# Kernel optimization log

Measured on AMD Instinct MI355X. Metric: run time of the kernel, lower is better.

The kernel has to match this reference:

```python
import jax, jax.numpy as jnp
import numpy as np

B, T, N, C, H = 32, 50, 1024, 128, 64


def setup_inputs() -> dict:
    key = jax.random.key(0)
    ks = jax.random.split(key, 5)
    s_ih = 1.0 / np.sqrt(H)
    return {
        "chars": jax.random.normal(ks[0], (B, T, N, C), dtype=jnp.float32),
        "W_ih": jax.random.uniform(ks[1], (3 * H, C), minval=-s_ih, maxval=s_ih, dtype=jnp.float32),
        "W_hh": jax.random.uniform(ks[2], (3 * H, H), minval=-s_ih, maxval=s_ih, dtype=jnp.float32),
        "b_ih": jax.random.uniform(ks[3], (3 * H,), minval=-s_ih, maxval=s_ih, dtype=jnp.float32),
        "b_hh": jax.random.uniform(ks[4], (3 * H,), minval=-s_ih, maxval=s_ih, dtype=jnp.float32),
    }


def _gru_scan(chars, W_ih, W_hh, b_ih, b_hh):
    b, t, n, c = chars.shape
    h_dim = W_hh.shape[1]
    # (B,T,N,C) -> (T, B*N, C): every (batch, stock) pair is an independent sequence
    x = jnp.transpose(chars, (1, 0, 2, 3)).reshape(t, b * n, c)
    # precompute input projections for all steps: (T, B*N, 3H)
    gi = jnp.einsum("tbc,gc->tbg", x, W_ih) + b_ih

    def step(h, gi_t):
        gh = h @ W_hh.T + b_hh                      # (B*N, 3H)
        i_r, i_z, i_n = jnp.split(gi_t, 3, axis=-1)
        h_r, h_z, h_n = jnp.split(gh, 3, axis=-1)
        r = jax.nn.sigmoid(i_r + h_r)
        z = jax.nn.sigmoid(i_z + h_z)
        nn_ = jnp.tanh(i_n + r * h_n)
        h_new = (1.0 - z) * nn_ + z * h
        return h_new, None

    h0 = jnp.zeros((b * n, h_dim), dtype=chars.dtype)
    h_final, _ = jax.lax.scan(step, h0, gi)
    return h_final.reshape(b, n, h_dim)


def reference(chars, W_ih, W_hh, b_ih, b_hh):
    return _gru_scan(chars, W_ih, W_hh, b_ih, b_hh)
```

## Files before the change

kernel.cpp:

```cpp
#include <hip/hip_runtime.h>


typedef _Float16 half8 __attribute__((ext_vector_type(8)));
typedef float f32x4 __attribute__((ext_vector_type(4)));

constexpr int T_ = 50, N_ = 1024, C_ = 128, H_ = 64;
constexpr uint32_t WIH_OFF = 0;
constexpr uint32_t HT_OFF  = 49152;
constexpr int LDS_BYTES = 57344;

__global__ void prep_weights(const float* __restrict__ Wih, const float* __restrict__ Whh,
                             _Float16* __restrict__ w16) {
  int i = blockIdx.x * 256 + threadIdx.x;
  if (i < 192 * 128) w16[i] = (_Float16)Wih[i];
  if (i < 192 * 64)  w16[24576 + i] = (_Float16)Whh[i];
}

__device__ __forceinline__ float sigm(float x) {
  return __builtin_amdgcn_rcpf(1.f + __expf(-x));
}

__global__ __launch_bounds__(256, 2) void gru_phase(
    const float* __restrict__ x, const _Float16* __restrict__ w16,
    const float* __restrict__ bih, const float* __restrict__ bhh,
    float* __restrict__ out)
{
  __shared__ __align__(16) char lds[LDS_BYTES];
  const int tid = threadIdx.x;

  {
#pragma unroll
    for (int rep = 0; rep < 12; ++rep) {
      int i = tid + rep * 256;
      int row = i >> 4;
      uint32_t byte = ((uint32_t)i << 4) ^ ((uint32_t)(row & 7) << 4);
      *(half8*)(lds + WIH_OFF + byte) = *(const half8*)(w16 + i * 8);
    }
    half8 zz = {};
    *(half8*)(lds + HT_OFF + tid * 32)      = zz;
    *(half8*)(lds + HT_OFF + tid * 32 + 16) = zz;
  }
  __syncthreads();

  const int wv = tid >> 6, lane = tid & 63;
  const int c = lane & 15, g = lane >> 4;
  const int sw7 = c & 7;
  const uint32_t ht = HT_OFF + (uint32_t)wv * 2048;
  const int seq0 = blockIdx.x * 64 + wv * 16;
  const int b = seq0 >> 10, n0 = seq0 & (N_ - 1);

  const _Float16* whh = w16 + 24576;
  half8 wf[3][4][2];
#pragma unroll
  for (int gate = 0; gate < 3; ++gate)
#pragma unroll
    for (int jt = 0; jt < 4; ++jt)
#pragma unroll
      for (int ks2 = 0; ks2 < 2; ++ks2)
        wf[gate][jt][ks2] =
            *(const half8*)(whh + (gate * 64 + jt * 16 + c) * 64 + ks2 * 32 + g * 8);

  float br[4], bz[4], bin_[4], bhn_[4];
#pragma unroll
  for (int jt = 0; jt < 4; ++jt) {
    int j = jt * 16 + c;
    br[jt]   = bih[j] + bhh[j];
    bz[jt]   = bih[64 + j] + bhh[64 + j];
    bin_[jt] = bih[128 + j];
    bhn_[jt] = bhh[128 + j];
  }

  float hr[16];
#pragma unroll
  for (int i = 0; i < 16; ++i) hr[i] = 0.f;

  const float* xlane = x + ((size_t)b * T_ * N_ + n0 + c) * C_ + g * 8;
  const size_t stepstride = (size_t)N_ * C_;

#define WIHB(gate, jt, ks) \
  (*(const half8*)(lds + WIH_OFF + (uint32_t)((((gate) * 64 + (jt) * 16 + c)) * 256) + \
                   (uint32_t)((((ks) * 4 + g) ^ sw7) << 4)))
#define MFMA16(a, bf, acc) __builtin_amdgcn_mfma_f32_16x16x32_f16((a), (bf), (acc), 0, 0, 0)

  float4 raw[8];
#pragma unroll
  for (int ks = 0; ks < 4; ++ks) {
    raw[ks * 2]     = *(const float4*)(xlane + ks * 32);
    raw[ks * 2 + 1] = *(const float4*)(xlane + ks * 32 + 4);
  }

  for (int t = 0; t < T_; ++t) {
    half8 xf[4];
#pragma unroll
    for (int ks = 0; ks < 4; ++ks) {
      const float4 lo = raw[ks * 2], hi = raw[ks * 2 + 1];
      half8 v;
      v[0] = (_Float16)lo.x; v[1] = (_Float16)lo.y;
      v[2] = (_Float16)lo.z; v[3] = (_Float16)lo.w;
      v[4] = (_Float16)hi.x; v[5] = (_Float16)hi.y;
      v[6] = (_Float16)hi.z; v[7] = (_Float16)hi.w;
      xf[ks] = v;
    }
    {
      const int tn = (t + 1 < T_) ? t + 1 : T_ - 1;
      const float* xp = xlane + (size_t)tn * stepstride;
#pragma unroll
      for (int ks = 0; ks < 4; ++ks) {
        raw[ks * 2]     = *(const float4*)(xp + ks * 32);
        raw[ks * 2 + 1] = *(const float4*)(xp + ks * 32 + 4);
      }
    }
    half8 ha[2];
#pragma unroll
    for (int ks2 = 0; ks2 < 2; ++ks2)
      ha[ks2] = *(const half8*)(lds + ht + (uint32_t)c * 128 +
                                (uint32_t)(((ks2 * 4 + g) ^ sw7) << 4));

#pragma unroll
    for (int jt = 0; jt < 4; ++jt) {
      f32x4 aR = {0.f, 0.f, 0.f, 0.f}, aZ = {0.f, 0.f, 0.f, 0.f};
      f32x4 aN = {0.f, 0.f, 0.f, 0.f}, aH = {0.f, 0.f, 0.f, 0.f};
#pragma unroll
      for (int ks = 0; ks < 4; ++ks) {
        const half8 a = xf[ks];
        aR = MFMA16(a, WIHB(0, jt, ks), aR);
        aZ = MFMA16(a, WIHB(1, jt, ks), aZ);
        aN = MFMA16(a, WIHB(2, jt, ks), aN);
      }
#pragma unroll
      for (int ks2 = 0; ks2 < 2; ++ks2) {
        const half8 a = ha[ks2];
        aR = MFMA16(a, wf[0][jt][ks2], aR);
        aZ = MFMA16(a, wf[1][jt][ks2], aZ);
        aH = MFMA16(a, wf[2][jt][ks2], aH);
      }
#pragma unroll
      for (int v = 0; v < 4; ++v) {
        const float r = sigm(aR[v] + br[jt]);
        const float z = sigm(aZ[v] + bz[jt]);
        const float np = aN[v] + bin_[jt] + r * (aH[v] + bhn_[jt]);
        const float nn = 1.f - 2.f * __builtin_amdgcn_rcpf(__expf(2.f * np) + 1.f);
        const float hn = (1.f - z) * nn + z * hr[jt * 4 + v];
        hr[jt * 4 + v] = hn;
        const int seq = g * 4 + v;
        const uint32_t gr = (uint32_t)((jt * 2 + (c >> 3)) ^ (seq & 7));
        const uint32_t byte = ht + (uint32_t)seq * 128 + (gr << 4) + (uint32_t)((c & 7) * 2);
        *(_Float16*)(lds + byte) = (_Float16)hn;
      }
    }
  }

#pragma unroll
  for (int jt = 0; jt < 4; ++jt)
#pragma unroll
    for (int v = 0; v < 4; ++v)
      out[(size_t)(seq0 + g * 4 + v) * H_ + jt * 16 + c] = hr[jt * 4 + v];
#undef WIHB
#undef MFMA16
}

extern "C" void kernel_launch(void* const* d_in, const int* in_sizes, int n_in,
                              void* d_out, int out_size, void* d_ws, size_t ws_size,
                              hipStream_t stream) {
  const float* chars = (const float*)d_in[0];
  const float* Wih   = (const float*)d_in[1];
  const float* Whh   = (const float*)d_in[2];
  const float* bih   = (const float*)d_in[3];
  const float* bhh   = (const float*)d_in[4];

  _Float16* w16 = (_Float16*)d_ws;

  prep_weights<<<96, 256, 0, stream>>>(Wih, Whh, w16);
  gru_phase<<<512, 256, 0, stream>>>(chars, w16, bih, bhh, (float*)d_out);
}
```

Baseline: 224.7 us.

## Split hidden dimension across waves, sharing one 16-sequence tile per block

```diff
diff --git a/kernel.cpp b/kernel.cpp
--- a/kernel.cpp
+++ b/kernel.cpp
@@ -5,9 +5,10 @@
 typedef float f32x4 __attribute__((ext_vector_type(4)));
 
 constexpr int T_ = 50, N_ = 1024, C_ = 128, H_ = 64;
-constexpr uint32_t WIH_OFF = 0;
-constexpr uint32_t HT_OFF  = 49152;
-constexpr int LDS_BYTES = 57344;
+constexpr uint32_t WHH_OFF = 0;
+constexpr uint32_t XB_OFF  = 24576;
+constexpr uint32_t HB_OFF  = 32768;
+constexpr int LDS_BYTES = 36864;
 
 __global__ void prep_weights(const float* __restrict__ Wih, const float* __restrict__ Whh,
                              _Float16* __restrict__ w16) {
@@ -20,142 +21,136 @@
   return __builtin_amdgcn_rcpf(1.f + __expf(-x));
 }
 
-__global__ __launch_bounds__(256, 2) void gru_phase(
+__device__ __forceinline__ half8 cvt8(float4 lo, float4 hi) {
+  half8 v;
+  v[0] = (_Float16)lo.x; v[1] = (_Float16)lo.y;
+  v[2] = (_Float16)lo.z; v[3] = (_Float16)lo.w;
+  v[4] = (_Float16)hi.x; v[5] = (_Float16)hi.y;
+  v[6] = (_Float16)hi.z; v[7] = (_Float16)hi.w;
+  return v;
+}
+
+__global__ __launch_bounds__(256, 4) void gru_g4(
     const float* __restrict__ x, const _Float16* __restrict__ w16,
     const float* __restrict__ bih, const float* __restrict__ bhh,
     float* __restrict__ out)
 {
   __shared__ __align__(16) char lds[LDS_BYTES];
   const int tid = threadIdx.x;
+  const int wv = tid >> 6, lane = tid & 63;
+  const int c = lane & 15, g = lane >> 4;
+  const int jt = wv;
+  const int seq0 = blockIdx.x * 16;
+  const int b = seq0 >> 10, n0 = seq0 & (N_ - 1);
 
   {
+    const _Float16* whh = w16 + 24576;
 #pragma unroll
-    for (int rep = 0; rep < 12; ++rep) {
+    for (int rep = 0; rep < 6; ++rep) {
       int i = tid + rep * 256;
-      int row = i >> 4;
-      uint32_t byte = ((uint32_t)i << 4) ^ ((uint32_t)(row & 7) << 4);
-      *(half8*)(lds + WIH_OFF + byte) = *(const half8*)(w16 + i * 8);
+      int row = i >> 3, gr = i & 7;
+      uint32_t byte = (uint32_t)row * 128 + (uint32_t)((gr ^ (row & 7)) << 4);
+      *(half8*)(lds + WHH_OFF + byte) = *(const half8*)(whh + i * 8);
     }
     half8 zz = {};
-    *(half8*)(lds + HT_OFF + tid * 32)      = zz;
-    *(half8*)(lds + HT_OFF + tid * 32 + 16) = zz;
+    *(half8*)(lds + HB_OFF + tid * 16) = zz;
   }
-  __syncthreads();
 
-  const int wv = tid >> 6, lane = tid & 63;
-  const int c = lane & 15, g = lane >> 4;
-  const int sw7 = c & 7;
-  const uint32_t ht = HT_OFF + (uint32_t)wv * 2048;
-  const int seq0 = blockIdx.x * 64 + wv * 16;
-  const int b = seq0 >> 10, n0 = seq0 & (N_ - 1);
-
-  const _Float16* whh = w16 + 24576;
-  half8 wf[3][4][2];
+  half8 wr[3][4];
 #pragma unroll
   for (int gate = 0; gate < 3; ++gate)
 #pragma unroll
-    for (int jt = 0; jt < 4; ++jt)
-#pragma unroll
-      for (int ks2 = 0; ks2 < 2; ++ks2)
-        wf[gate][jt][ks2] =
-            *(const half8*)(whh + (gate * 64 + jt * 16 + c) * 64 + ks2 * 32 + g * 8);
+    for (int ks = 0; ks < 4; ++ks)
+      wr[gate][ks] = *(const half8*)(w16 + (gate * 64 + jt * 16 + c) * 128 + ks * 32 + g * 8);
 
-  float br[4], bz[4], bin_[4], bhn_[4];
-#pragma unroll
-  for (int jt = 0; jt < 4; ++jt) {
-    int j = jt * 16 + c;
-    br[jt]   = bih[j] + bhh[j];
-    bz[jt]   = bih[64 + j] + bhh[64 + j];
-    bin_[jt] = bih[128 + j];
-    bhn_[jt] = bhh[128 + j];
-  }
+  const int j = jt * 16 + c;
+  const float br   = bih[j] + bhh[j];
+  const float bz   = bih[64 + j] + bhh[64 + j];
+  const float bin_ = bih[128 + j];
+  const float bhn_ = bhh[128 + j];
 
-  float hr[16];
-#pragma unroll
-  for (int i = 0; i < 16; ++i) hr[i] = 0.f;
+  float hr[4] = {0.f, 0.f, 0.f, 0.f};
 
-  const float* xlane = x + ((size_t)b * T_ * N_ + n0 + c) * C_ + g * 8;
+  const int sseq = tid >> 4;
+  const uint32_t xw_off = (uint32_t)sseq * 256 +
+                          (uint32_t)(((tid & 15) ^ (sseq & 7)) << 4);
+  const float* xbase = x + ((size_t)b * T_ * N_ + n0 + sseq) * C_ + (tid & 15) * 8;
   const size_t stepstride = (size_t)N_ * C_;
 
-#define WIHB(gate, jt, ks) \
-  (*(const half8*)(lds + WIH_OFF + (uint32_t)((((gate) * 64 + (jt) * 16 + c)) * 256) + \
-                   (uint32_t)((((ks) * 4 + g) ^ sw7) << 4)))
+#define WHHB(gate, ks2) \
+  (*(const half8*)(lds + WHH_OFF + (uint32_t)(((gate) * 64 + jt * 16 + c) * 128) + \
+                   (uint32_t)((((ks2) * 4 + g) ^ (c & 7)) << 4)))
 #define MFMA16(a, bf, acc) __builtin_amdgcn_mfma_f32_16x16x32_f16((a), (bf), (acc), 0, 0, 0)
 
-  float4 raw[8];
-#pragma unroll
-  for (int ks = 0; ks < 4; ++ks) {
-    raw[ks * 2]     = *(const float4*)(xlane + ks * 32);
-    raw[ks * 2 + 1] = *(const float4*)(xlane + ks * 32 + 4);
+  {
+    float4 r0 = *(const float4*)(xbase);
+    float4 r1 = *(const float4*)(xbase + 4);
+    *(half8*)(lds + XB_OFF + xw_off) = cvt8(r0, r1);
   }
+  float4 ra = *(const float4*)(xbase + stepstride);
+  float4 rb = *(const float4*)(xbase + stepstride + 4);
+  __syncthreads();
 
   for (int t = 0; t < T_; ++t) {
-    half8 xf[4];
+    const uint32_t xr  = XB_OFF + (uint32_t)(t & 1) * 4096;
+    const uint32_t hrd = HB_OFF + (uint32_t)((t + 1) & 1) * 2048;
+    const uint32_t hwr = HB_OFF + (uint32_t)(t & 1) * 2048;
+
+    half8 xa[4];
 #pragma unroll
-    for (int ks = 0; ks < 4; ++ks) {
-      const float4 lo = raw[ks * 2], hi = raw[ks * 2 + 1];
-      half8 v;
-      v[0] = (_Float16)lo.x; v[1] = (_Float16)lo.y;
-      v[2] = (_Float16)lo.z; v[3] = (_Float16)lo.w;
-      v[4] = (_Float16)hi.x; v[5] = (_Float16)hi.y;
-      v[6] = (_Float16)hi.z; v[7] = (_Float16)hi.w;
-      xf[ks] = v;
-    }
-    {
-      const int tn = (t + 1 < T_) ? t + 1 : T_ - 1;
-      const float* xp = xlane + (size_t)tn * stepstride;
-#pragma unroll
-      for (int ks = 0; ks < 4; ++ks) {
-        raw[ks * 2]     = *(const float4*)(xp + ks * 32);
-        raw[ks * 2 + 1] = *(const float4*)(xp + ks * 32 + 4);
-      }
-    }
+    for (int ks = 0; ks < 4; ++ks)
+      xa[ks] = *(const half8*)(lds + xr + (uint32_t)c * 256 +
+                               (uint32_t)(((ks * 4 + g) ^ (c & 7)) << 4));
     half8 ha[2];
 #pragma unroll
     for (int ks2 = 0; ks2 < 2; ++ks2)
-      ha[ks2] = *(const half8*)(lds + ht + (uint32_t)c * 128 +
-                                (uint32_t)(((ks2 * 4 + g) ^ sw7) << 4));
+      ha[ks2] = *(const half8*)(lds + hrd + (uint32_t)c * 128 +
+                                (uint32_t)(((ks2 * 4 + g) ^ (c & 7)) << 4));
+
+    f32x4 aR = {0.f, 0.f, 0.f, 0.f}, aZ = {0.f, 0.f, 0.f, 0.f};
+    f32x4 aN = {0.f, 0.f, 0.f, 0.f}, aH = {0.f, 0.f, 0.f, 0.f};
 
 #pragma unroll
-    for (int jt = 0; jt < 4; ++jt) {
-      f32x4 aR = {0.f, 0.f, 0.f, 0.f}, aZ = {0.f, 0.f, 0.f, 0.f};
-      f32x4 aN = {0.f, 0.f, 0.f, 0.f}, aH = {0.f, 0.f, 0.f, 0.f};
+    for (int ks = 0; ks < 4; ++ks) {
+      aR = MFMA16(xa[ks], wr[0][ks], aR);
+      aZ = MFMA16(xa[ks], wr[1][ks], aZ);
+      aN = MFMA16(xa[ks], wr[2][ks], aN);
+    }
 #pragma unroll
-      for (int ks = 0; ks < 4; ++ks) {
-        const half8 a = xf[ks];
-        aR = MFMA16(a, WIHB(0, jt, ks), aR);
-        aZ = MFMA16(a, WIHB(1, jt, ks), aZ);
-        aN = MFMA16(a, WIHB(2, jt, ks), aN);
-      }
+    for (int ks2 = 0; ks2 < 2; ++ks2) {
+      aR = MFMA16(ha[ks2], WHHB(0, ks2), aR);
+      aZ = MFMA16(ha[ks2], WHHB(1, ks2), aZ);
+      aH = MFMA16(ha[ks2], WHHB(2, ks2), aH);
+    }
+
 #pragma unroll
-      for (int ks2 = 0; ks2 < 2; ++ks2) {
-        const half8 a = ha[ks2];
-        aR = MFMA16(a, wf[0][jt][ks2], aR);
-        aZ = MFMA16(a, wf[1][jt][ks2], aZ);
-        aH = MFMA16(a, wf[2][jt][ks2], aH);
-      }
-#pragma unroll
-      for (int v = 0; v < 4; ++v) {
-        const float r = sigm(aR[v] + br[jt]);
-        const float z = sigm(aZ[v] + bz[jt]);
-        const float np = aN[v] + bin_[jt] + r * (aH[v] + bhn_[jt]);
-        const float nn = 1.f - 2.f * __builtin_amdgcn_rcpf(__expf(2.f * np) + 1.f);
-        const float hn = (1.f - z) * nn + z * hr[jt * 4 + v];
-        hr[jt * 4 + v] = hn;
-        const int seq = g * 4 + v;
-        const uint32_t gr = (uint32_t)((jt * 2 + (c >> 3)) ^ (seq & 7));
-        const uint32_t byte = ht + (uint32_t)seq * 128 + (gr << 4) + (uint32_t)((c & 7) * 2);
-        *(_Float16*)(lds + byte) = (_Float16)hn;
-      }
+    for (int v = 0; v < 4; ++v) {
+      const float r = sigm(aR[v] + br);
+      const float z = sigm(aZ[v] + bz);
+      const float np = aN[v] + bin_ + r * (aH[v] + bhn_);
+      const float nn = 1.f - 2.f * __builtin_amdgcn_rcpf(__expf(2.f * np) + 1.f);
+      const float hn = (1.f - z) * nn + z * hr[v];
+      hr[v] = hn;
+      const int seq = g * 4 + v;
+      const uint32_t gr = (uint32_t)((jt * 2 + (c >> 3)) ^ (seq & 7));
+      *(_Float16*)(lds + hwr + (uint32_t)seq * 128 + (gr << 4) +
+                   (uint32_t)((c & 7) * 2)) = (_Float16)hn;
     }
+
+    if (t + 1 < T_) {
+      *(half8*)(lds + XB_OFF + (uint32_t)((t + 1) & 1) * 4096 + xw_off) = cvt8(ra, rb);
+      const int tn2 = (t + 2 < T_) ? t + 2 : T_ - 1;
+      const float* xp = xbase + (size_t)tn2 * stepstride;
+      ra = *(const float4*)(xp);
+      rb = *(const float4*)(xp + 4);
+    }
+    __syncthreads();
   }
 
 #pragma unroll
-  for (int jt = 0; jt < 4; ++jt)
-#pragma unroll
-    for (int v = 0; v < 4; ++v)
-      out[(size_t)(seq0 + g * 4 + v) * H_ + jt * 16 + c] = hr[jt * 4 + v];
-#undef WIHB
+  for (int v = 0; v < 4; ++v)
+    out[(size_t)(seq0 + g * 4 + v) * H_ + j] = hr[v];
+#undef WHHB
 #undef MFMA16
 }
 
@@ -171,5 +166,5 @@
   _Float16* w16 = (_Float16*)d_ws;
 
   prep_weights<<<96, 256, 0, stream>>>(Wih, Whh, w16);
-  gru_phase<<<512, 256, 0, stream>>>(chars, w16, bih, bhh, (float*)d_out);
+  gru_g4<<<2048, 256, 0, stream>>>(chars, w16, bih, bhh, (float*)d_out);
 }
```

After: 216.2 us. -3.8%, faster.
